# Kernel tuning notes

Measured on AMD Instinct MI355X. Metric: run time of the kernel, lower is better.

Reference implementation:

```python
import jax, jax.numpy as jnp
import numpy as np

D_MODEL = 96
D_STATE = 16
D_INNER = 192   # expand * d_model
DT_RANK = 6     # ceil(96/16)
D_DEPTH_OUT = 1024  # (64/2)*(64/2)
BATCH, HH, WW = 2, 64, 64


def silu(v):
    return v * jax.nn.sigmoid(v)


def setup_inputs() -> dict:
    key = jax.random.key(0)
    ks = jax.random.split(key, 10)
    f = jnp.float32
    x = jax.random.normal(ks[0], (BATCH, HH, WW, D_MODEL), f)
    in_proj_w = jax.random.normal(ks[1], (2 * D_INNER, D_MODEL), f) * 0.02
    conv2d_w = jax.random.normal(ks[2], (D_INNER, 1, 3, 3), f) * 0.1  # depthwise, groups=D_INNER
    conv2d_b = jnp.zeros((D_INNER,), f)
    depth_conv_w = jax.random.normal(ks[3], (D_INNER, 1, 3, 3), f) * 0.1  # depthwise, stride 2
    depth_conv_b = jnp.zeros((D_INNER,), f)
    depth_fc_w = jax.random.normal(ks[4], (D_INNER, D_DEPTH_OUT), f) * 0.02
    depth_fc_b = jnp.zeros((D_INNER,), f)
    x_proj_w = jax.random.normal(ks[5], (DT_RANK + 2 * D_STATE, D_INNER), f) * 0.02
    dt_init_std = DT_RANK ** (-0.5)
    dt_projs_w = jax.random.uniform(ks[6], (D_INNER, DT_RANK), f, -dt_init_std, dt_init_std)
    # inverse-softplus of dt ~ U(log 1e-3, log 0.1)
    dt = jnp.exp(jax.random.uniform(ks[7], (D_INNER,), f) * (np.log(0.1) - np.log(0.001)) + np.log(0.001))
    dt = jnp.clip(dt, 1e-4, None)
    dt_projs_b = dt + jnp.log(-jnp.expm1(-dt))
    A_logs = jnp.log(jnp.tile(jnp.arange(1, D_STATE + 1, dtype=f)[None, :], (D_INNER, 1)))
    Ds = jnp.ones((D_INNER,), f)
    out_norm_w = jnp.ones((D_INNER,), f)
    out_norm_b = jnp.zeros((D_INNER,), f)
    out_proj_w = jax.random.normal(ks[8], (D_MODEL, D_INNER), f) * 0.02
    return dict(x=x, in_proj_w=in_proj_w, conv2d_w=conv2d_w, conv2d_b=conv2d_b,
                depth_conv_w=depth_conv_w, depth_conv_b=depth_conv_b,
                depth_fc_w=depth_fc_w, depth_fc_b=depth_fc_b, x_proj_w=x_proj_w,
                dt_projs_w=dt_projs_w, dt_projs_b=dt_projs_b, A_logs=A_logs, Ds=Ds,
                out_norm_w=out_norm_w, out_norm_b=out_norm_b, out_proj_w=out_proj_w)


def _selective_scan(u, delta, A, Bm, Cm, D, delta_bias):
    # u, delta: [B, D, L]; A: [D, N]; Bm, Cm: [B, N, L]; D: [D]; delta_bias: [D]
    delta = jax.nn.softplus(delta + delta_bias[None, :, None])
    dA = jnp.exp(jnp.einsum('bdl,dn->lbdn', delta, A))          # [L,B,D,N]
    dBu = jnp.einsum('bdl,bnl,bdl->lbdn', delta, Bm, u)          # [L,B,D,N]
    Ct = jnp.transpose(Cm, (2, 0, 1))                            # [L,B,N]
    h0 = jnp.zeros(dA.shape[1:], u.dtype)

    def step(h, inp):
        a, b, c = inp
        h = a * h + b                                            # S6 recurrence
        return h, jnp.einsum('bdn,bn->bd', h, c)

    _, ys = jax.lax.scan(step, h0, (dA, dBu, Ct))                # ys: [L,B,D]
    y = jnp.transpose(ys, (1, 2, 0))                             # [B,D,L]
    return y + D[None, :, None] * u


def _forward(x, in_proj_w, conv2d_w, conv2d_b, depth_conv_w, depth_conv_b,
             depth_fc_w, depth_fc_b, x_proj_w, dt_projs_w, dt_projs_b,
             A_logs, Ds, out_norm_w, out_norm_b, out_proj_w):
    B, H, W, _ = x.shape
    Di, N, R = D_INNER, D_STATE, DT_RANK
    dn = ('NCHW', 'OIHW', 'NCHW')
    xz = x @ in_proj_w.T
    x1, z = jnp.split(xz, 2, axis=-1)
    xc = jnp.transpose(x1, (0, 3, 1, 2))                         # [B,Di,H,W]
    xc = jax.lax.conv_general_dilated(xc, conv2d_w, (1, 1), [(1, 1), (1, 1)],
                                      dimension_numbers=dn, feature_group_count=Di)
    xc = silu(xc + conv2d_b[None, :, None, None])
    dxc = jax.lax.conv_general_dilated(xc, depth_conv_w, (2, 2), [(1, 1), (1, 1)],
                                       dimension_numbers=dn, feature_group_count=Di)
    dxc = dxc + depth_conv_b[None, :, None, None]                # [B,Di,H/2,W/2]
    dx = dxc.reshape(B, Di, -1)                                  # [B,Di,1024]
    dx = dx @ depth_fc_w.T + depth_fc_b                          # [B,Di,Di]
    dx = silu(jnp.transpose(dx, (0, 2, 1)))                      # [B,Di,CC], CC=Di
    L = H * W
    CC = dx.shape[-1]
    xs = jnp.concatenate([dx, xc.reshape(B, Di, L)], axis=-1)    # mode='head': [B,Di,LL]
    x_dbl = jnp.einsum('bdl,cd->bcl', xs, x_proj_w)
    dts, Bm, Cm = x_dbl[:, :R], x_dbl[:, R:R + N], x_dbl[:, R + N:]
    dts = jnp.einsum('brl,dr->bdl', dts, dt_projs_w)
    A = -jnp.exp(A_logs)
    y = _selective_scan(xs, dts, A, Bm, Cm, Ds, dt_projs_b)
    y = y[..., CC:]                                              # drop depth tokens (head mode)
    y = jnp.transpose(y, (0, 2, 1)).reshape(B, H, W, Di)
    mu = jnp.mean(y, axis=-1, keepdims=True)
    var = jnp.var(y, axis=-1, keepdims=True)
    y = (y - mu) * jax.lax.rsqrt(var + 1e-5) * out_norm_w + out_norm_b
    y = y * silu(z)
    return y @ out_proj_w.T


def reference(x, in_proj_w, conv2d_w, conv2d_b, depth_conv_w, depth_conv_b,
              depth_fc_w, depth_fc_b, x_proj_w, dt_projs_w, dt_projs_b,
              A_logs, Ds, out_norm_w, out_norm_b, out_proj_w):
    return _forward(x, in_proj_w, conv2d_w, conv2d_b, depth_conv_w, depth_conv_b,
                    depth_fc_w, depth_fc_b, x_proj_w, dt_projs_w, dt_projs_b,
                    A_logs, Ds, out_norm_w, out_norm_b, out_proj_w)
```

## Files before the change

kernel.cpp:

```cpp
#include <hip/hip_runtime.h>
#include <hip/hip_bf16.h>

typedef __hip_bfloat16 bf16;

#define BATCH 2
#define DM 96
#define DI 192
#define LSP 4096
#define LD 192
#define LTOT 4288
#define NST 16
#define RK 6
#define DFC 1024
#define CLEN 64
#define NCH 67
#define SCH 64
#define XR 16
#define NG  (BATCH * DI * NST)

__device__ __forceinline__ float b2f(bf16 v) { return __bfloat162float(v); }
__device__ __forceinline__ float silu_f(float x) { return x / (1.f + __expf(-x)); }
__device__ __forceinline__ float softplus_f(float x) { return x > 20.f ? x : log1pf(__expf(x)); }

__device__ __forceinline__ int is_f32(const void* alog) {
    return ((const unsigned int*)alog)[0] == 0u;
}
__device__ __forceinline__ float LDI(const void* p, int i, int f32m) {
    return f32m ? ((const float*)p)[i] : __bfloat162float(((const bf16*)p)[i]);
}
__device__ __forceinline__ void unpack2(unsigned int u, float* o) {
    o[0] = __uint_as_float(u << 16);
    o[1] = __uint_as_float(u & 0xffff0000u);
}

__device__ __forceinline__ float row16_sum(float v) {
    v += __int_as_float(__builtin_amdgcn_update_dpp(0, __float_as_int(v), 0x128, 0xf, 0xf, true));
    v += __int_as_float(__builtin_amdgcn_update_dpp(0, __float_as_int(v), 0x124, 0xf, 0xf, true));
    v += __int_as_float(__builtin_amdgcn_update_dpp(0, __float_as_int(v), 0x122, 0xf, 0xf, true));
    v += __int_as_float(__builtin_amdgcn_update_dpp(0, __float_as_int(v), 0x121, 0xf, 0xf, true));
    return v;
}

#define TW(r, i)  ((r) * 64 + ((((i) >> 2) + (r)) & 15) * 4 + ((i) & 3))

__global__ __launch_bounds__(256) void k_wprep(const void* __restrict__ ipw, float* __restrict__ wT,
                                               const void* __restrict__ alog) {
    const int f32m = is_f32(alog);
    int idx = blockIdx.x * 256 + threadIdx.x;
    if (idx < 96 * 384) {
        int k = idx / 384, c = idx - k * 384;
        wT[idx] = LDI(ipw, c * 96 + k, f32m);
    }
}

__global__ __launch_bounds__(384) void k_inproj2(const void* __restrict__ x, const float* __restrict__ wT,
                                                 float* __restrict__ x1, float* __restrict__ z,
                                                 const void* __restrict__ alog) {
    __shared__ __align__(16) float sx[16 * 100];
    const int f32m = is_f32(alog);
    int t = threadIdx.x;
    int row0 = blockIdx.x * 16;
    {
        int e = t * 4;
        int row = e / 96, k = e - row * 96;
        float4 v;
        if (f32m) {
            v = *((const float4*)((const float*)x + (row0 + row) * 96 + k));
        } else {
            uint2 u = *((const uint2*)((const ushort*)x + (row0 + row) * 96 + k));
            float f[4];
            unpack2(u.x, &f[0]); unpack2(u.y, &f[2]);
            v = make_float4(f[0], f[1], f[2], f[3]);
        }
        *(float4*)&sx[row * 100 + k] = v;
    }
    __syncthreads();
    int rg = t / 96, cg = t - rg * 96;
    int c0 = cg * 4, rbase = rg * 4;
    float acc[4][4];
    #pragma unroll
    for (int r = 0; r < 4; r++)
        #pragma unroll
        for (int cc = 0; cc < 4; cc++) acc[r][cc] = 0.f;
    const float* wp = wT + c0;
    #pragma unroll 4
    for (int k4 = 0; k4 < 24; k4++) {
        float4 xv[4], wv[4];
        #pragma unroll
        for (int r = 0; r < 4; r++) xv[r] = *(const float4*)&sx[(rbase + r) * 100 + k4 * 4];
        #pragma unroll
        for (int q = 0; q < 4; q++) wv[q] = *(const float4*)&wp[(k4 * 4 + q) * 384];
        #pragma unroll
        for (int r = 0; r < 4; r++) {
            float xr[4] = {xv[r].x, xv[r].y, xv[r].z, xv[r].w};
            #pragma unroll
            for (int q = 0; q < 4; q++) {
                acc[r][0] += xr[q] * wv[q].x;
                acc[r][1] += xr[q] * wv[q].y;
                acc[r][2] += xr[q] * wv[q].z;
                acc[r][3] += xr[q] * wv[q].w;
            }
        }
    }
    #pragma unroll
    for (int r = 0; r < 4; r++) {
        int row = row0 + rbase + r;
        float4 o = make_float4(acc[r][0], acc[r][1], acc[r][2], acc[r][3]);
        if (c0 < DI) *(float4*)&x1[row * DI + c0] = o;
        else         *(float4*)&z[row * DI + (c0 - DI)] = o;
    }
}

__global__ __launch_bounds__(192) void k_conv1(const float* __restrict__ x1, const void* __restrict__ cw,
                                               const void* __restrict__ cb, float* __restrict__ xs,
                                               const void* __restrict__ alog) {
    const int f32m = is_f32(alog);
    int d = threadIdx.x;
    int blk = blockIdx.x;
    int b = blk >> 9;
    int rest = blk & 511;
    int h = rest >> 3, w0 = (rest & 7) * 8;
    float wgt[9];
    #pragma unroll
    for (int i = 0; i < 9; i++) wgt[i] = LDI(cw, d * 9 + i, f32m);
    float bias = LDI(cb, d, f32m);
    float val[3][10];
    #pragma unroll
    for (int dh = 0; dh < 3; dh++) {
        int hh = h + dh - 1;
        #pragma unroll
        for (int j = 0; j < 10; j++) {
            int ww = w0 + j - 1;
            val[dh][j] = ((unsigned)hh < 64u && (unsigned)ww < 64u)
                       ? x1[((b << 12) + (hh << 6) + ww) * DI + d] : 0.f;
        }
    }
    #pragma unroll
    for (int i = 0; i < 8; i++) {
        float acc = bias;
        #pragma unroll
        for (int dh = 0; dh < 3; dh++)
            #pragma unroll
            for (int dw = 0; dw < 3; dw++)
                acc += val[dh][i + dw] * wgt[dh * 3 + dw];
        xs[(b * LTOT + LD + (h << 6) + w0 + i) * DI + d] = silu_f(acc);
    }
}

__global__ __launch_bounds__(192) void k_conv2(const float* __restrict__ xs, const void* __restrict__ dw,
                                               const void* __restrict__ db, float* __restrict__ dxc,
                                               const void* __restrict__ alog) {
    const int f32m = is_f32(alog);
    int d = threadIdx.x;
    int blk = blockIdx.x;
    int b = blk >> 10, lp = blk & 1023;
    int hp = lp >> 5, wp = lp & 31;
    float acc = LDI(db, d, f32m);
    #pragma unroll
    for (int dh = 0; dh < 3; dh++) {
        int h = 2 * hp + dh - 1;
        if ((unsigned)h >= 64u) continue;
        #pragma unroll
        for (int dw_ = 0; dw_ < 3; dw_++) {
            int w_ = 2 * wp + dw_ - 1;
            if ((unsigned)w_ >= 64u) continue;
            acc += xs[(b * LTOT + LD + (h << 6) + w_) * DI + d] * LDI(dw, d * 9 + dh * 3 + dw_, f32m);
        }
    }
    dxc[(b * DFC + lp) * DI + d] = acc;
}

__global__ __launch_bounds__(192) void k_dfc(const float* __restrict__ dxc, const void* __restrict__ fw,
                                             float* __restrict__ part, const void* __restrict__ alog) {
    __shared__ float sfw[4 * 128];
    const int f32m = is_f32(alog);
    int t = threadIdx.x;
    int blk = blockIdx.x;
    int p = blk / 96;
    int rem = blk - p * 96;
    int b   = rem / 48;
    int ch0 = (rem % 48) * 4;
    int k0  = p * 128;
    for (int idx = t; idx < 4 * 128; idx += 192)
        sfw[idx] = LDI(fw, (ch0 + (idx >> 7)) * DFC + k0 + (idx & 127), f32m);
    __syncthreads();
    float a0 = 0.f, a1 = 0.f, a2 = 0.f, a3 = 0.f;
    #pragma unroll 8
    for (int k = 0; k < 128; k++) {
        float dv = dxc[(b * DFC + k0 + k) * DI + t];
        a0 += dv * sfw[k];
        a1 += dv * sfw[128 + k];
        a2 += dv * sfw[256 + k];
        a3 += dv * sfw[384 + k];
    }
    int ob = ((p * 2 + b) * 192 + t) * DI + ch0;
    *(float4*)&part[ob] = make_float4(a0, a1, a2, a3);
}

__global__ __launch_bounds__(256) void k_xdbl(const float* __restrict__ xs_r, float* __restrict__ xs_w,
                                              const float* __restrict__ part, const void* __restrict__ fb,
                                              const void* __restrict__ xpw,
                                              float* __restrict__ BCb, float* __restrict__ dts,
                                              const void* __restrict__ alog) {
    __shared__ float sw[38 * 196];
    __shared__ float srow[XR][196];
    const int f32m = is_f32(alog);
    int t = threadIdx.x;
    for (int c = t >> 3; c < 38; c += 32) {
        int seg = (t & 7) * 24;
        for (int k = seg; k < seg + 24; k++) sw[c * 196 + k] = LDI(xpw, c * DI + k, f32m);
    }
    int row0 = blockIdx.x * XR;
    int bb = row0 >= LTOT ? 1 : 0;
    int depth = (row0 - bb * LTOT) < LD;
    for (int idx = t; idx < XR * DI; idx += 256) {
        int row = idx / DI, k = idx - row * DI;
        int grow = row0 + row;
        float v;
        if (depth) {
            int tok = grow - bb * LTOT;
            int o = (bb * 192 + tok) * DI + k;
            v = 0.f;
            #pragma unroll
            for (int p = 0; p < 8; p++) v += part[o + p * 73728];
            v = silu_f(v + LDI(fb, k, f32m));
            xs_w[grow * DI + k] = v;
        } else {
            v = xs_r[grow * DI + k];
        }
        srow[row][k] = v;
    }
    __syncthreads();
    int r = t & 15, cg = t >> 4;
    float a0 = 0.f, a1 = 0.f, a2 = 0.f;
    const float4* w0 = (const float4*)&sw[cg * 196];
    const float4* w1 = (const float4*)&sw[(cg + 16) * 196];
    const float4* w2 = (const float4*)&sw[(cg < 6 ? cg + 32 : cg) * 196];
    const float4* xr = (const float4*)&srow[r][0];
    #pragma unroll 4
    for (int k = 0; k < 48; k++) {
        float4 xv = xr[k], v0 = w0[k], v1 = w1[k], v2 = w2[k];
        a0 += xv.x * v0.x + xv.y * v0.y + xv.z * v0.z + xv.w * v0.w;
        a1 += xv.x * v1.x + xv.y * v1.y + xv.z * v1.z + xv.w * v1.w;
        a2 += xv.x * v2.x + xv.y * v2.y + xv.z * v2.z + xv.w * v2.w;
    }
    int grow = row0 + r;
    if (cg < 6) dts[grow * 6 + cg] = a0;
    else        BCb[grow * 32 + (cg - 6)] = a0;
    BCb[grow * 32 + (cg + 10)] = a1;
    if (cg < 6) BCb[grow * 32 + (cg + 26)] = a2;
}

__device__ __forceinline__ void delta_block_T(const float* sdts, const float* sdwb, float* sdel, int t) {
    int e = t * 4;
    int i = e >> 4, dl = e & 15;
    #pragma unroll
    for (int q = 0; q < 4; q++) {
        int r = dl + q;
        float dv = sdwb[96 + r];
        #pragma unroll
        for (int r2 = 0; r2 < RK; r2++) dv += sdts[i * RK + r2] * sdwb[r * RK + r2];
        sdel[TW(r, i)] = softplus_f(dv);
    }
}

__global__ __launch_bounds__(256) void k_scan1(const float* __restrict__ dts, const float* __restrict__ xs,
                                               const float* __restrict__ BCb, const void* __restrict__ dtw,
                                               const void* __restrict__ dtb, const void* __restrict__ alog,
                                               float2* __restrict__ AH) {
    __shared__ __align__(16) float su[1024];
    __shared__ __align__(16) float sB[1024];
    __shared__ __align__(16) float sdel[1024];
    __shared__ float sdts[CLEN * RK];
    __shared__ float sdwb[112];
    const int f32m = is_f32(alog);
    int t = threadIdx.x;
    int beta = blockIdx.x;
    int b = beta / (12 * NCH);
    int rem = beta - b * (12 * NCH);
    int dblk = rem / NCH, ch = rem - dblk * NCH;
    int d0 = dblk * 16, l0 = ch * CLEN;
    int bL = b * LTOT;
    {
        int e = t * 4;
        int i = e >> 4, dd = e & 15;
        float4 uv = *(const float4*)&xs[(bL + l0 + i) * DI + d0 + dd];
        float4 bv = *(const float4*)&BCb[(bL + l0 + i) * 32 + dd];
        float uu[4] = {uv.x, uv.y, uv.z, uv.w};
        float vb[4] = {bv.x, bv.y, bv.z, bv.w};
        #pragma unroll
        for (int q = 0; q < 4; q++) {
            int w = TW(dd + q, i);
            su[w] = uu[q];
            sB[w] = vb[q];
        }
    }
    for (int idx = t; idx < CLEN * RK; idx += 256) sdts[idx] = dts[(bL + l0) * RK + idx];
    if (t < 96)            sdwb[t] = LDI(dtw, (d0 + t / 6) * RK + (t % 6), f32m);
    else if (t < 112)      sdwb[t] = LDI(dtb, d0 + (t - 96), f32m);
    __syncthreads();
    delta_block_T(sdts, sdwb, sdel, t);
    __syncthreads();
    int dloc = t >> 4, n = t & 15;
    int d = d0 + dloc;
    float A = -__expf(LDI(alog, d * NST + n, f32m));
    float h = 0.f, ap = 1.f;
    int bd = dloc * 64, bn = n * 64;
    #pragma unroll
    for (int i4 = 0; i4 < 16; i4++) {
        int od = bd + (((i4 + dloc) & 15) << 2);
        int on = bn + (((i4 + n) & 15) << 2);
        float de[4], uu[4], vb[4];
        *(float4*)de = *(const float4*)&sdel[od];
        *(float4*)uu = *(const float4*)&su[od];
        *(float4*)vb = *(const float4*)&sB[on];
        #pragma unroll
        for (int q = 0; q < 4; q++) {
            float a = __expf(de[q] * A);
            h = a * h + de[q] * vb[q] * uu[q];
            ap *= a;
        }
    }
    int g = ((b * DI + d) * NST) + n;
    AH[ch * NG + g] = make_float2(ap, h);
}

__global__ __launch_bounds__(64) void k_scan2(const float2* __restrict__ AH, float* __restrict__ He) {
    int g = blockIdx.x * 64 + threadIdx.x;
    float h = 0.f;
    for (int ch = 0; ch < NCH; ch++) {
        He[ch * NG + g] = h;
        float2 v = AH[ch * NG + g];
        h = v.x * h + v.y;
    }
}

__global__ __launch_bounds__(256) void k_scan3(const float* __restrict__ dts, const float* __restrict__ xs,
                                               const float* __restrict__ BCb, const void* __restrict__ dtw,
                                               const void* __restrict__ dtb, const void* __restrict__ alog,
                                               const void* __restrict__ Dsv, const float* __restrict__ He,
                                               float* __restrict__ y) {
    __shared__ __align__(16) float su[1024];
    __shared__ __align__(16) float sbc[2048];
    __shared__ __align__(16) float sdel[1024];
    __shared__ float sdts[CLEN * RK];
    __shared__ float sdwb[112];
    const int f32m = is_f32(alog);
    int t = threadIdx.x;
    int beta = blockIdx.x;
    int b = beta / (12 * SCH);
    int rem = beta - b * (12 * SCH);
    int dblk = rem / SCH, ch = (rem - dblk * SCH) + 3;
    int d0 = dblk * 16, l0 = ch * CLEN;
    int bL = b * LTOT;
    {
        int e = t * 4;
        int i = e >> 4, dd = e & 15;
        float4 uv = *(const float4*)&xs[(bL + l0 + i) * DI + d0 + dd];
        float uu[4] = {uv.x, uv.y, uv.z, uv.w};
        #pragma unroll
        for (int q = 0; q < 4; q++) su[TW(dd + q, i)] = uu[q];
    }
    #pragma unroll
    for (int q2 = 0; q2 < 2; q2++) {
        int e = (t + q2 * 256) * 4;
        int i = e >> 5, c = e & 31;
        float4 v = *(const float4*)&BCb[(bL + l0 + i) * 32 + c];
        float vv[4] = {v.x, v.y, v.z, v.w};
        #pragma unroll
        for (int q = 0; q < 4; q++) sbc[TW(c + q, i)] = vv[q];
    }
    for (int idx = t; idx < CLEN * RK; idx += 256) sdts[idx] = dts[(bL + l0) * RK + idx];
    if (t < 96)            sdwb[t] = LDI(dtw, (d0 + t / 6) * RK + (t % 6), f32m);
    else if (t < 112)      sdwb[t] = LDI(dtb, d0 + (t - 96), f32m);
    __syncthreads();
    delta_block_T(sdts, sdwb, sdel, t);
    __syncthreads();
    int dloc = t >> 4, n = t & 15;
    int d = d0 + dloc;
    float A = -__expf(LDI(alog, d * NST + n, f32m));
    float Dv = LDI(Dsv, d, f32m);
    int g = ((b * DI + d) * NST) + n;
    float h = He[ch * NG + g];
    int bd = dloc * 64, bn = n * 64;
    #pragma unroll
    for (int i4 = 0; i4 < 16; i4++) {
        int od = bd + (((i4 + dloc) & 15) << 2);
        int on = bn + (((i4 + n) & 15) << 2);
        float de[4], uu[4], vb[4], vc[4];
        *(float4*)de = *(const float4*)&sdel[od];
        *(float4*)uu = *(const float4*)&su[od];
        *(float4*)vb = *(const float4*)&sbc[on];
        *(float4*)vc = *(const float4*)&sbc[on + 1024];
        #pragma unroll
        for (int q = 0; q < 4; q++) {
            float a = __expf(de[q] * A);
            h = a * h + de[q] * vb[q] * uu[q];
            float yv = row16_sum(h * vc[q]);
            if (n == 0) {
                int l = l0 + i4 * 4 + q;
                y[(b * LSP + (l - LD)) * DI + d] = yv + Dv * uu[q];
            }
        }
    }
}

__global__ __launch_bounds__(384) void k_out(const float* __restrict__ y, const float* __restrict__ z,
                                             const void* __restrict__ nw, const void* __restrict__ nb,
                                             const void* __restrict__ opw, void* __restrict__ out,
                                             const void* __restrict__ alog) {
    __shared__ float sg[2][DI];
    __shared__ float sred[2][2][3];
    const int f32m = is_f32(alog);
    int t = threadIdx.x;
    int m = t >> 2, kh = t & 3;
    float wr[48];
    if (f32m) {
        const float4* wp = (const float4*)((const float*)opw + m * DI + kh * 48);
        #pragma unroll
        for (int i = 0; i < 12; i++) {
            float4 v = wp[i];
            wr[4*i] = v.x; wr[4*i+1] = v.y; wr[4*i+2] = v.z; wr[4*i+3] = v.w;
        }
    } else {
        const uint4* wp = (const uint4*)((const bf16*)opw + m * DI + kh * 48);
        #pragma unroll
        for (int i = 0; i < 6; i++) {
            uint4 v = wp[i];
            unpack2(v.x, &wr[8*i]);   unpack2(v.y, &wr[8*i+2]);
            unpack2(v.z, &wr[8*i+4]); unpack2(v.w, &wr[8*i+6]);
        }
    }
    float nwv = 0.f, nbv = 0.f;
    if (t < DI) { nwv = LDI(nw, t, f32m); nbv = LDI(nb, t, f32m); }
    int wv_ = t >> 6;
    int row0 = blockIdx.x * 16;
    for (int pr = 0; pr < 8; pr++) {
        int r0 = row0 + pr * 2, r1 = r0 + 1;
        float y0 = 0.f, z0 = 0.f, y1 = 0.f, z1 = 0.f;
        if (t < DI) {
            y0 = y[r0 * DI + t]; z0 = z[r0 * DI + t];
            y1 = y[r1 * DI + t]; z1 = z[r1 * DI + t];
            float s0 = y0, q0 = y0 * y0, s1 = y1, q1 = y1 * y1;
            #pragma unroll
            for (int off = 32; off; off >>= 1) {
                s0 += __shfl_xor(s0, off); q0 += __shfl_xor(q0, off);
                s1 += __shfl_xor(s1, off); q1 += __shfl_xor(q1, off);
            }
            if ((t & 63) == 0) {
                sred[0][0][wv_] = s0; sred[0][1][wv_] = q0;
                sred[1][0][wv_] = s1; sred[1][1][wv_] = q1;
            }
        }
        __syncthreads();
        if (t < DI) {
            float S0  = sred[0][0][0] + sred[0][0][1] + sred[0][0][2];
            float Q0  = sred[0][1][0] + sred[0][1][1] + sred[0][1][2];
            float S1  = sred[1][0][0] + sred[1][0][1] + sred[1][0][2];
            float Q1  = sred[1][1][0] + sred[1][1][1] + sred[1][1][2];
            float mu0 = S0 * (1.f / 192.f), var0 = Q0 * (1.f / 192.f) - mu0 * mu0;
            float mu1 = S1 * (1.f / 192.f), var1 = Q1 * (1.f / 192.f) - mu1 * mu1;
            float g0 = (y0 - mu0) * rsqrtf(var0 + 1e-5f) * nwv + nbv;
            g0 *= z0 / (1.f + __expf(-z0));
            float g1 = (y1 - mu1) * rsqrtf(var1 + 1e-5f) * nwv + nbv;
            g1 *= z1 / (1.f + __expf(-z1));
            sg[0][t] = g0;
            sg[1][t] = g1;
        }
        __syncthreads();
        const float* g0p = &sg[0][kh * 48];
        const float* g1p = &sg[1][kh * 48];
        float a0 = 0.f, a1 = 0.f;
        #pragma unroll
        for (int j = 0; j < 48; j++) {
            a0 += g0p[j] * wr[j];
            a1 += g1p[j] * wr[j];
        }
        a0 += __shfl_xor(a0, 1); a0 += __shfl_xor(a0, 2);
        a1 += __shfl_xor(a1, 1); a1 += __shfl_xor(a1, 2);
        if (kh == 0) {
            if (f32m) {
                ((float*)out)[r0 * DM + m] = a0;
                ((float*)out)[r1 * DM + m] = a1;
            } else {
                ((bf16*)out)[r0 * DM + m] = __float2bfloat16(a0);
                ((bf16*)out)[r1 * DM + m] = __float2bfloat16(a1);
            }
        }
    }
}

extern "C" void kernel_launch(void* const* d_in, const int* in_sizes, int n_in,
                              void* d_out, int out_size, void* d_ws, size_t ws_size,
                              hipStream_t stream) {
    (void)in_sizes; (void)n_in; (void)out_size; (void)ws_size;
    const void* x    = d_in[0];
    const void* ipw  = d_in[1];
    const void* c1w  = d_in[2];
    const void* c1b  = d_in[3];
    const void* c2w  = d_in[4];
    const void* c2b  = d_in[5];
    const void* fcw  = d_in[6];
    const void* fcb  = d_in[7];
    const void* xpw  = d_in[8];
    const void* dtw  = d_in[9];
    const void* dtb  = d_in[10];
    const void* alog = d_in[11];
    const void* Dsv  = d_in[12];
    const void* nw   = d_in[13];
    const void* nb   = d_in[14];
    const void* opw  = d_in[15];

    float* ws  = (float*)d_ws;
    float* x1  = ws;
    float* z   = x1  + BATCH * LSP * DI;
    float* xs  = z   + BATCH * LSP * DI;
    float* dxc = xs  + BATCH * LTOT * DI;
    float* BCb = dxc + BATCH * DFC * DI;
    float* dts = BCb + BATCH * LTOT * 32;
    float2* AH = (float2*)(dts + BATCH * LTOT * RK);
    float* He  = (float*)(AH + NCH * NG);
    float* wT  = He + NCH * NG;
    float* part = x1;
    float* y    = x1;

    k_wprep  <<<dim3(144), dim3(256), 0, stream>>>(ipw, wT, alog);
    k_inproj2<<<dim3(512), dim3(384), 0, stream>>>(x, wT, x1, z, alog);
    k_conv1  <<<dim3(1024), dim3(DI), 0, stream>>>(x1, c1w, c1b, xs, alog);
    k_conv2  <<<dim3(BATCH * DFC), dim3(DI), 0, stream>>>(xs, c2w, c2b, dxc, alog);
    k_dfc    <<<dim3(768), dim3(DI), 0, stream>>>(dxc, fcw, part, alog);
    k_xdbl   <<<dim3(536), dim3(256), 0, stream>>>(xs, xs, part, fcb, xpw, BCb, dts, alog);
    k_scan1  <<<dim3(BATCH * 12 * NCH), dim3(256), 0, stream>>>(dts, xs, BCb, dtw, dtb, alog, AH);
    k_scan2  <<<dim3(96), dim3(64), 0, stream>>>(AH, He);
    k_scan3  <<<dim3(BATCH * 12 * SCH), dim3(256), 0, stream>>>(dts, xs, BCb, dtw, dtb, alog, Dsv, He, y);
    k_out    <<<dim3(512), dim3(384), 0, stream>>>(y, z, nw, nb, opw, d_out, alog);
}
```

Measured before the change: 221.8 us.

## Fuse depthwise conv and strided depth conv into one kernel

Merges the 3x3 depthwise conv+SiLU kernel and the stride-2 depth conv kernel into a single kernel. Each block computes a 2x8 tile of conv1 output plus a halo (recomputing halo rows/columns), writes the interior to xs, and uses the in-register conv1 values to produce 4 depth-conv outputs. This removes one launch and the re-read of xs from global memory, at the cost of redundant halo recompute, more registers, and half as many blocks.

```diff
diff --git a/kernel.cpp b/kernel.cpp
--- a/kernel.cpp
+++ b/kernel.cpp
@@ -18,7 +18,6 @@
 #define XR 16
 #define NG  (BATCH * DI * NST)
 
-__device__ __forceinline__ float b2f(bf16 v) { return __bfloat162float(v); }
 __device__ __forceinline__ float silu_f(float x) { return x / (1.f + __expf(-x)); }
 __device__ __forceinline__ float softplus_f(float x) { return x > 20.f ? x : log1pf(__expf(x)); }
 
@@ -111,63 +110,70 @@
     }
 }
 
-__global__ __launch_bounds__(192) void k_conv1(const float* __restrict__ x1, const void* __restrict__ cw,
-                                               const void* __restrict__ cb, float* __restrict__ xs,
-                                               const void* __restrict__ alog) {
+__global__ __launch_bounds__(192) void k_conv12(const float* __restrict__ x1, const void* __restrict__ cw,
+                                                const void* __restrict__ cb, const void* __restrict__ dw,
+                                                const void* __restrict__ db, float* __restrict__ xs,
+                                                float* __restrict__ dxc, const void* __restrict__ alog) {
     const int f32m = is_f32(alog);
     int d = threadIdx.x;
     int blk = blockIdx.x;
-    int b = blk >> 9;
-    int rest = blk & 511;
-    int h = rest >> 3, w0 = (rest & 7) * 8;
-    float wgt[9];
-    #pragma unroll
-    for (int i = 0; i < 9; i++) wgt[i] = LDI(cw, d * 9 + i, f32m);
-    float bias = LDI(cb, d, f32m);
-    float val[3][10];
-    #pragma unroll
-    for (int dh = 0; dh < 3; dh++) {
-        int hh = h + dh - 1;
-        #pragma unroll
-        for (int j = 0; j < 10; j++) {
-            int ww = w0 + j - 1;
-            val[dh][j] = ((unsigned)hh < 64u && (unsigned)ww < 64u)
-                       ? x1[((b << 12) + (hh << 6) + ww) * DI + d] : 0.f;
-        }
-    }
-    #pragma unroll
-    for (int i = 0; i < 8; i++) {
-        float acc = bias;
-        #pragma unroll
-        for (int dh = 0; dh < 3; dh++)
+    int b = blk >> 8;
+    int rest = blk & 255;
+    int hp = rest >> 3, wt = rest & 7;
+    float wgt1[9], wgt2[9];
+    #pragma unroll
+    for (int i = 0; i < 9; i++) { wgt1[i] = LDI(cw, d * 9 + i, f32m); wgt2[i] = LDI(dw, d * 9 + i, f32m); }
+    float bias1 = LDI(cb, d, f32m);
+    float bias2 = LDI(db, d, f32m);
+    float val[5][11];
+    #pragma unroll
+    for (int r = 0; r < 5; r++) {
+        int hh = 2 * hp - 2 + r;
+        #pragma unroll
+        for (int j = 0; j < 11; j++) {
+            int ww = 8 * wt - 2 + j;
+            val[r][j] = ((unsigned)hh < 64u && (unsigned)ww < 64u)
+                      ? x1[((b << 12) + (hh << 6) + ww) * DI + d] : 0.f;
+        }
+    }
+    float c1[3][9];
+    #pragma unroll
+    for (int rr = 0; rr < 3; rr++) {
+        #pragma unroll
+        for (int i = 0; i < 9; i++) {
+            float acc = bias1;
             #pragma unroll
-            for (int dw = 0; dw < 3; dw++)
-                acc += val[dh][i + dw] * wgt[dh * 3 + dw];
-        xs[(b * LTOT + LD + (h << 6) + w0 + i) * DI + d] = silu_f(acc);
-    }
-}
-
-__global__ __launch_bounds__(192) void k_conv2(const float* __restrict__ xs, const void* __restrict__ dw,
-                                               const void* __restrict__ db, float* __restrict__ dxc,
-                                               const void* __restrict__ alog) {
-    const int f32m = is_f32(alog);
-    int d = threadIdx.x;
-    int blk = blockIdx.x;
-    int b = blk >> 10, lp = blk & 1023;
-    int hp = lp >> 5, wp = lp & 31;
-    float acc = LDI(db, d, f32m);
-    #pragma unroll
-    for (int dh = 0; dh < 3; dh++) {
-        int h = 2 * hp + dh - 1;
-        if ((unsigned)h >= 64u) continue;
-        #pragma unroll
-        for (int dw_ = 0; dw_ < 3; dw_++) {
-            int w_ = 2 * wp + dw_ - 1;
-            if ((unsigned)w_ >= 64u) continue;
-            acc += xs[(b * LTOT + LD + (h << 6) + w_) * DI + d] * LDI(dw, d * 9 + dh * 3 + dw_, f32m);
-        }
-    }
-    dxc[(b * DFC + lp) * DI + d] = acc;
+            for (int dh = 0; dh < 3; dh++)
+                #pragma unroll
+                for (int dw_ = 0; dw_ < 3; dw_++)
+                    acc += val[rr + dh][i + dw_] * wgt1[dh * 3 + dw_];
+            c1[rr][i] = silu_f(acc);
+        }
+    }
+    #pragma unroll
+    for (int rr = 1; rr < 3; rr++) {
+        int row = 2 * hp + (rr - 1);
+        #pragma unroll
+        for (int i = 1; i < 9; i++) {
+            int wa = 8 * wt + (i - 1);
+            xs[(b * LTOT + LD + (row << 6) + wa) * DI + d] = c1[rr][i];
+        }
+    }
+    #pragma unroll
+    for (int wpl = 0; wpl < 4; wpl++) {
+        int wpa = 4 * wt + wpl;
+        float acc = bias2;
+        #pragma unroll
+        for (int dh = 0; dh < 3; dh++) {
+            if (2 * hp + dh - 1 < 0) continue;
+            #pragma unroll
+            for (int dw_ = 0; dw_ < 3; dw_++) {
+                if (2 * wpa + dw_ - 1 < 0) continue;
+                acc += c1[dh][2 * wpl + dw_] * wgt2[dh * 3 + dw_];
+            }
+        }
+        dxc[(b * DFC + hp * 32 + wpa) * DI + d] = acc;
+    }
 }
 
 __global__ __launch_bounds__(192) void k_dfc(const float* __restrict__ dxc, const void* __restrict__ fw,
@@ -526,8 +532,7 @@
 
     k_wprep  <<<dim3(144), dim3(256), 0, stream>>>(ipw, wT, alog);
     k_inproj2<<<dim3(512), dim3(384), 0, stream>>>(x, wT, x1, z, alog);
-    k_conv1  <<<dim3(1024), dim3(DI), 0, stream>>>(x1, c1w, c1b, xs, alog);
-    k_conv2  <<<dim3(BATCH * DFC), dim3(DI), 0, stream>>>(xs, c2w, c2b, dxc, alog);
+    k_conv12 <<<dim3(512), dim3(DI), 0, stream>>>(x1, c1w, c1b, c2w, c2b, xs, dxc, alog);
     k_dfc    <<<dim3(768), dim3(DI), 0, stream>>>(dxc, fcw, part, alog);
     k_xdbl   <<<dim3(536), dim3(256), 0, stream>>>(xs, xs, part, fcb, xpw, BCb, dts, alog);
     k_scan1  <<<dim3(BATCH * 12 * NCH), dim3(256), 0, stream>>>(dts, xs, BCb, dtw, dtb, alog, AH);
```

New measurement: 217.6 us (median of 2 runs). About the same (-1.9%).
